# Performance work log

Measured on AMD Instinct MI355X. Metric: run time of the kernel, lower is better.

## Reference

```python
import jax, jax.numpy as jnp
import numpy as np

N = 50000      # nodes
E = 800000     # edges (before self-loops)
NFEAT = 128
NHID = 32
H = 8
NCLASS = 47
NEG_SLOPE = 0.2  # PyG GATv2Conv default


def gatv2_layer(x, src, dst, Wl, Wr, att, b, n):
    """One GATv2Conv layer (concat over heads). att: [H, C]."""
    h, c = att.shape
    xl = (x @ Wl).reshape(n, h, c)  # source transform (lin_l)
    xr = (x @ Wr).reshape(n, h, c)  # target transform (lin_r)
    e = jax.nn.leaky_relu(xl[src] + xr[dst], NEG_SLOPE)   # [E, H, C]
    logits = jnp.einsum('ehc,hc->eh', e, att)             # [E, H]
    # segment softmax over incoming edges of each target node
    m = jax.ops.segment_max(logits, dst, num_segments=n)  # [N, H]
    alpha = jnp.exp(logits - m[dst])
    denom = jax.ops.segment_sum(alpha, dst, num_segments=n)
    alpha = alpha / (denom[dst] + 1e-16)
    msg = xl[src] * alpha[:, :, None]                     # [E, H, C]
    out = jax.ops.segment_sum(msg, dst, num_segments=n)   # [N, H, C]
    return out.reshape(n, h * c) + b


def setup_inputs():
    key = jax.random.key(0)
    ks = jax.random.split(key, 16)
    s = 0.1
    x = jax.random.normal(ks[0], (N, NFEAT), jnp.float32)
    edge_index = jax.random.randint(ks[1], (2, E), 0, N)
    HID = H * NHID  # 256
    params = dict(
        Wl0=jax.random.normal(ks[2], (NFEAT, HID), jnp.float32) * s,
        Wr0=jax.random.normal(ks[3], (NFEAT, HID), jnp.float32) * s,
        a0=jax.random.normal(ks[4], (H, NHID), jnp.float32) * s,
        b0=jnp.zeros((HID,), jnp.float32),
        Wl1=jax.random.normal(ks[5], (HID, HID), jnp.float32) * s,
        Wr1=jax.random.normal(ks[6], (HID, HID), jnp.float32) * s,
        a1=jax.random.normal(ks[7], (H, NHID), jnp.float32) * s,
        b1=jnp.zeros((HID,), jnp.float32),
        Wl2=jax.random.normal(ks[8], (HID, NCLASS), jnp.float32) * s,
        Wr2=jax.random.normal(ks[9], (HID, NCLASS), jnp.float32) * s,
        a2=jax.random.normal(ks[10], (1, NCLASS), jnp.float32) * s,
        b2=jnp.zeros((NCLASS,), jnp.float32),
    )
    return {"x": x, "edge_index": edge_index, **params}


def reference(x, edge_index, Wl0, Wr0, a0, b0, Wl1, Wr1, a1, b1, Wl2, Wr2, a2, b2):
    n = x.shape[0]
    # PyG GATv2Conv adds self-loops by default
    loops = jnp.arange(n, dtype=edge_index.dtype)
    src = jnp.concatenate([edge_index[0], loops])
    dst = jnp.concatenate([edge_index[1], loops])
    h = gatv2_layer(x, src, dst, Wl0, Wr0, a0, b0, n)
    h = jax.nn.elu(h)
    h = gatv2_layer(h, src, dst, Wl1, Wr1, a1, b1, n)
    h = jax.nn.elu(h)
    h = gatv2_layer(h, src, dst, Wl2, Wr2, a2, b2, n)
    return jax.nn.log_softmax(h, axis=-1)
```

## Files before the change

### kernel.cpp

```cpp
#include <hip/hip_runtime.h>
#include <cmath>


#define NFEAT 128
#define HID 256
#define NCLS 47
#define L2PAD 64
#define LOG2E 1.44269504088896340736f

typedef __attribute__((ext_vector_type(8))) short bf16x8;
typedef __attribute__((ext_vector_type(4))) float f32x4;
typedef __attribute__((ext_vector_type(2))) float f32x2;

__device__ __forceinline__ unsigned short f2b(float f) {
  unsigned int u = __builtin_bit_cast(unsigned int, f);
  u += 0x7FFFu + ((u >> 16) & 1u);
  return (unsigned short)(u >> 16);
}
__device__ __forceinline__ float b2f(unsigned short s) {
  return __builtin_bit_cast(float, (unsigned int)s << 16);
}
__device__ __forceinline__ f32x2 b2f2(unsigned int u) {
  return (f32x2){__builtin_bit_cast(float, u << 16),
                 __builtin_bit_cast(float, u & 0xFFFF0000u)};
}
__device__ __forceinline__ void glds16(const unsigned short* g, unsigned short* l) {
  __builtin_amdgcn_global_load_lds(
      (const __attribute__((address_space(1))) unsigned int*)g,
      (__attribute__((address_space(3))) unsigned int*)l, 16, 0, 0);
}

__device__ __forceinline__ float quad_sum(float v) {
  int t = __builtin_amdgcn_mov_dpp(__builtin_bit_cast(int, v), 0xB1, 0xF, 0xF, true);
  v += __builtin_bit_cast(float, t);
  t = __builtin_amdgcn_mov_dpp(__builtin_bit_cast(int, v), 0x4E, 0xF, 0xF, true);
  v += __builtin_bit_cast(float, t);
  return v;
}

struct WtArgs {
  const float* W[6];
  unsigned short* WT[6];
  int K[6], M[6], off[6], total;
  const float* att;
  float* att48;
  int* deg;
  int n;
};
__global__ void k_wt_all(WtArgs a) {
  int i = blockIdx.x * blockDim.x + threadIdx.x;
  if (i >= a.total) {
    int j = i - a.total;
    if (j < 48) { a.att48[j] = (j < NCLS) ? a.att[j] * LOG2E : 0.f; return; }
    j -= 48;
    if (j < a.n) a.deg[j] = 1;
    return;
  }
  int s = 0;
  #pragma unroll
  for (int j = 1; j < 6; ++j) if (i >= a.off[j]) s = j;
  int jj = i - a.off[s];
  int K = a.K[s], M = a.M[s];
  int m = jj / K, k = jj - m * K;
  a.WT[s][jj] = (m < M) ? f2b(a.W[s][(size_t)k * M + m]) : (unsigned short)0;
}

__global__ void k_cast_count(const float* __restrict__ in,
                             unsigned short* __restrict__ out, int n4,
                             const int* __restrict__ dst,
                             int* __restrict__ deg, int e) {
  int i = blockIdx.x * blockDim.x + threadIdx.x;
  if (i < n4) {
    float4 v = reinterpret_cast<const float4*>(in)[i];
    ushort4 o = {f2b(v.x), f2b(v.y), f2b(v.z), f2b(v.w)};
    reinterpret_cast<ushort4*>(out)[i] = o;
  } else {
    int j = i - n4;
    if (j < e) atomicAdd(&deg[dst[j]], 1);
  }
}

__global__ __launch_bounds__(256) void k_bsum(const int* __restrict__ deg,
                                              int* __restrict__ bsum, int n) {
  int t = threadIdx.x;
  int base = blockIdx.x * 1024 + t * 4;
  int s = 0;
  if (base + 3 < n) {
    int4 v = *reinterpret_cast<const int4*>(deg + base);
    s = v.x + v.y + v.z + v.w;
  } else {
    for (int j = 0; j < 4; ++j) { int i = base + j; if (i < n) s += deg[i]; }
  }
  #pragma unroll
  for (int off = 1; off < 64; off <<= 1) s += __shfl_xor(s, off, 64);
  __shared__ int wsum[4];
  if ((t & 63) == 0) wsum[t >> 6] = s;
  __syncthreads();
  if (t == 0) bsum[blockIdx.x] = wsum[0] + wsum[1] + wsum[2] + wsum[3];
}

__global__ void k_scanb(int* __restrict__ bsum, int nb) {
  int lane = threadIdx.x;
  int v = (lane < nb) ? bsum[lane] : 0;
  #pragma unroll
  for (int off = 1; off < 64; off <<= 1) {
    int u = __shfl_up(v, off, 64);
    if (lane >= off) v += u;
  }
  if (lane < nb) bsum[lane] = v;
}

__global__ __launch_bounds__(256) void k_scanfinal(const int* __restrict__ deg,
                                                   const int* __restrict__ bscan,
                                                   int* __restrict__ rowptr,
                                                   int2* __restrict__ csr,
                                                   int* __restrict__ cursor, int n) {
  int t = threadIdx.x, b = blockIdx.x;
  int base = b * 1024 + t * 4;
  int v0 = 0, v1 = 0, v2 = 0, v3 = 0;
  if (base + 3 < n) {
    int4 v = *reinterpret_cast<const int4*>(deg + base);
    v0 = v.x; v1 = v.y; v2 = v.z; v3 = v.w;
  } else {
    if (base < n) v0 = deg[base];
    if (base + 1 < n) v1 = deg[base + 1];
    if (base + 2 < n) v2 = deg[base + 2];
    if (base + 3 < n) v3 = deg[base + 3];
  }
  int s = v0 + v1 + v2 + v3;
  int incl = s;
  #pragma unroll
  for (int off = 1; off < 64; off <<= 1) {
    int u = __shfl_up(incl, off, 64);
    if ((t & 63) >= off) incl += u;
  }
  __shared__ int wsum[4];
  int w = t >> 6, l = t & 63;
  if (l == 63) wsum[w] = incl;
  __syncthreads();
  int woff = 0;
  for (int j = 0; j < w; ++j) woff += wsum[j];
  int excl = incl - s + woff;
  int boff = (b == 0) ? 0 : bscan[b - 1];
  int p0 = boff + excl;
  int p1 = p0 + v0, p2 = p1 + v1, p3 = p2 + v2, p4 = p3 + v3;
  if (base < n)     { rowptr[base + 1] = p1; csr[p0] = make_int2(base, base);         cursor[base]     = p0 + 1; }
  if (base + 1 < n) { rowptr[base + 2] = p2; csr[p1] = make_int2(base + 1, base + 1); cursor[base + 1] = p1 + 1; }
  if (base + 2 < n) { rowptr[base + 3] = p3; csr[p2] = make_int2(base + 2, base + 2); cursor[base + 2] = p2 + 1; }
  if (base + 3 < n) { rowptr[base + 4] = p4; csr[p3] = make_int2(base + 3, base + 3); cursor[base + 3] = p3 + 1; }
  if (b == 0 && t == 0) rowptr[0] = 0;
}

__global__ void k_scatter(const int* __restrict__ src, const int* __restrict__ dst,
                          int* __restrict__ cursor, int2* __restrict__ csr, int e) {
  int i = blockIdx.x * blockDim.x + threadIdx.x;
  if (i < e) {
    int d = dst[i];
    int p = atomicAdd(&cursor[d], 1);
    csr[p] = make_int2(src[i], d);
  }
}

__global__ __launch_bounds__(512) void gemm_dual_bf16_128(
    const unsigned short* __restrict__ X, const unsigned short* __restrict__ WlT,
    const unsigned short* __restrict__ WrT, unsigned short* __restrict__ XL,
    unsigned short* __restrict__ XR, int N, int K, int Mpad) {
  __shared__ __align__(16) unsigned short S[3 * 128 * 64];
  unsigned short* Xs = S;
  unsigned short* Ls = S + 8192;
  unsigned short* Rs = S + 16384;

  const int t = threadIdx.x;
  const int col0 = blockIdx.x * 128;
  const int row0 = blockIdx.y * 128;
  const int w = t >> 6, lane = t & 63;
  const int wr = w >> 2, wc = w & 3;
  const int r15 = lane & 15, kc = lane >> 4;
  const bool tail = (row0 + 128 > N);

  const int row_a = t >> 3,          c16_a = t & 7;
  const int row_b = (t + 512) >> 3,  c16_b = t & 7;
  const int sg_a = (c16_a ^ (row_a & 7)) * 8;
  const int sg_b = (c16_b ^ (row_b & 7)) * 8;
  unsigned short* d0 = S + w * 512;
  unsigned short* d1 = S + 4096 + w * 512;

  f32x4 accL[4][2], accR[4][2];
  #pragma unroll
  for (int rf = 0; rf < 4; ++rf)
    #pragma unroll
    for (int cf = 0; cf < 2; ++cf) {
      accL[rf][cf] = (f32x4){0.f, 0.f, 0.f, 0.f};
      accR[rf][cf] = (f32x4){0.f, 0.f, 0.f, 0.f};
    }

  for (int k0 = 0; k0 < K; k0 += 64) {
    glds16(WlT + (size_t)(col0 + row_a) * K + k0 + sg_a, d0 + 8192);
    glds16(WlT + (size_t)(col0 + row_b) * K + k0 + sg_b, d1 + 8192);
    glds16(WrT + (size_t)(col0 + row_a) * K + k0 + sg_a, d0 + 16384);
    glds16(WrT + (size_t)(col0 + row_b) * K + k0 + sg_b, d1 + 16384);
    if (!tail) {
      glds16(X + (size_t)(row0 + row_a) * K + k0 + sg_a, d0);
      glds16(X + (size_t)(row0 + row_b) * K + k0 + sg_b, d1);
    } else {
      uint4 va = (uint4){0, 0, 0, 0}, vb = (uint4){0, 0, 0, 0};
      if (row0 + row_a < N)
        va = *reinterpret_cast<const uint4*>(X + (size_t)(row0 + row_a) * K + k0 + sg_a);
      if (row0 + row_b < N)
        vb = *reinterpret_cast<const uint4*>(X + (size_t)(row0 + row_b) * K + k0 + sg_b);
      *reinterpret_cast<uint4*>(Xs + row_a * 64 + c16_a * 8) = va;
      *reinterpret_cast<uint4*>(Xs + row_b * 64 + c16_b * 8) = vb;
    }
    __syncthreads();

    #pragma unroll
    for (int ks = 0; ks < 2; ++ks) {
      const int c16 = ks * 4 + kc;
      bf16x8 a[4];
      #pragma unroll
      for (int rf = 0; rf < 4; ++rf) {
        const int rA = wr * 64 + rf * 16 + r15;
        a[rf] = *reinterpret_cast<const bf16x8*>(Xs + rA * 64 + ((c16 ^ (rA & 7)) * 8));
      }
      #pragma unroll
      for (int cf = 0; cf < 2; ++cf) {
        const int rB = wc * 32 + cf * 16 + r15;
        const int so = rB * 64 + ((c16 ^ (rB & 7)) * 8);
        const bf16x8 bl = *reinterpret_cast<const bf16x8*>(Ls + so);
        const bf16x8 br = *reinterpret_cast<const bf16x8*>(Rs + so);
        #pragma unroll
        for (int rf = 0; rf < 4; ++rf) {
          accL[rf][cf] = __builtin_amdgcn_mfma_f32_16x16x32_bf16(a[rf], bl, accL[rf][cf], 0, 0, 0);
          accR[rf][cf] = __builtin_amdgcn_mfma_f32_16x16x32_bf16(a[rf], br, accR[rf][cf], 0, 0, 0);
        }
      }
    }
    __syncthreads();
  }

  #pragma unroll
  for (int rf = 0; rf < 4; ++rf) {
    #pragma unroll
    for (int cf = 0; cf < 2; ++cf) {
      int cc = col0 + wc * 32 + cf * 16 + r15;
      #pragma unroll
      for (int i = 0; i < 4; ++i) {
        int rr = row0 + wr * 64 + rf * 16 + kc * 4 + i;
        if (rr < N) {
          XL[(size_t)rr * Mpad + cc] = f2b(accL[rf][cf][i]);
          XR[(size_t)rr * Mpad + cc] = f2b(accR[rf][cf][i]);
        }
      }
    }
  }
}

__global__ __launch_bounds__(256) void gemm_dual_bf16(
    const unsigned short* __restrict__ X, const unsigned short* __restrict__ WlT,
    const unsigned short* __restrict__ WrT, unsigned short* __restrict__ XL,
    unsigned short* __restrict__ XR, int N, int K, int Mpad) {
  __shared__ __align__(16) unsigned short S[3 * 64 * 64];
  unsigned short* Xs = S;
  unsigned short* Ls = S + 4096;
  unsigned short* Rs = S + 8192;

  const int t = threadIdx.x;
  const int col0 = blockIdx.x * 64;
  const int row0 = blockIdx.y * 64;
  const int w = t >> 6, lane = t & 63;
  const int r15 = lane & 15, kc = lane >> 4;
  const bool tail = (row0 + 64 > N);

  const int rowa = t >> 3, c16a = t & 7;
  const int rowb = (t + 256) >> 3, c16b = t & 7;
  const int sga = (c16a ^ (rowa & 7)) * 8;
  const int sgb = (c16b ^ (rowb & 7)) * 8;
  unsigned short* ldst0 = S + (w * 512);
  unsigned short* ldst1 = S + (2048 + w * 512);

  f32x4 accL[4], accR[4];
  #pragma unroll
  for (int i = 0; i < 4; ++i) {
    accL[i] = (f32x4){0.f, 0.f, 0.f, 0.f};
    accR[i] = (f32x4){0.f, 0.f, 0.f, 0.f};
  }

  const int rA = 16 * w + r15;

  for (int k0 = 0; k0 < K; k0 += 64) {
    glds16(WlT + (size_t)(col0 + rowa) * K + k0 + sga, ldst0 + 4096);
    glds16(WlT + (size_t)(col0 + rowb) * K + k0 + sgb, ldst1 + 4096);
    glds16(WrT + (size_t)(col0 + rowa) * K + k0 + sga, ldst0 + 8192);
    glds16(WrT + (size_t)(col0 + rowb) * K + k0 + sgb, ldst1 + 8192);
    if (!tail) {
      glds16(X + (size_t)(row0 + rowa) * K + k0 + sga, ldst0);
      glds16(X + (size_t)(row0 + rowb) * K + k0 + sgb, ldst1);
    } else {
      uint4 va = (uint4){0, 0, 0, 0}, vb = (uint4){0, 0, 0, 0};
      if (row0 + rowa < N)
        va = *reinterpret_cast<const uint4*>(X + (size_t)(row0 + rowa) * K + k0 + sga);
      if (row0 + rowb < N)
        vb = *reinterpret_cast<const uint4*>(X + (size_t)(row0 + rowb) * K + k0 + sgb);
      *reinterpret_cast<uint4*>(Xs + rowa * 64 + c16a * 8) = va;
      *reinterpret_cast<uint4*>(Xs + rowb * 64 + c16b * 8) = vb;
    }
    __syncthreads();

    #pragma unroll
    for (int ks = 0; ks < 2; ++ks) {
      const int c16 = ks * 4 + kc;
      const bf16x8 a = *reinterpret_cast<const bf16x8*>(
          Xs + rA * 64 + ((c16 ^ (rA & 7)) * 8));
      #pragma unroll
      for (int nf = 0; nf < 4; ++nf) {
        const int rB = nf * 16 + r15;
        const int so = rB * 64 + ((c16 ^ (rB & 7)) * 8);
        const bf16x8 bl = *reinterpret_cast<const bf16x8*>(Ls + so);
        const bf16x8 br = *reinterpret_cast<const bf16x8*>(Rs + so);
        accL[nf] = __builtin_amdgcn_mfma_f32_16x16x32_bf16(a, bl, accL[nf], 0, 0, 0);
        accR[nf] = __builtin_amdgcn_mfma_f32_16x16x32_bf16(a, br, accR[nf], 0, 0, 0);
      }
    }
    __syncthreads();
  }

  #pragma unroll
  for (int nf = 0; nf < 4; ++nf) {
    int cc = col0 + nf * 16 + r15;
    #pragma unroll
    for (int i = 0; i < 4; ++i) {
      int rr = row0 + 16 * w + kc * 4 + i;
      if (rr < N) {
        XL[(size_t)rr * Mpad + cc] = f2b(accL[nf][i]);
        XR[(size_t)rr * Mpad + cc] = f2b(accR[nf][i]);
      }
    }
  }
}

__global__ __launch_bounds__(256) void gat_node_hc(
    const unsigned short* __restrict__ xl, const unsigned short* __restrict__ xr,
    const float* __restrict__ att, const float* __restrict__ bias,
    const int* __restrict__ rowptr, const int2* __restrict__ csr,
    unsigned short* __restrict__ out, int n) {
  int wid = (blockIdx.x * blockDim.x + threadIdx.x) >> 6;
  int lane = threadIdx.x & 63;
  if (wid >= n) return;
  const int q = lane & 31, half = lane >> 5;

  const uint4 xrp = *reinterpret_cast<const uint4*>(xr + (size_t)wid * HID + q * 8);
  const f32x2 xr2[4] = {b2f2(xrp.x), b2f2(xrp.y), b2f2(xrp.z), b2f2(xrp.w)};
  const float4 af0 = *reinterpret_cast<const float4*>(att + q * 8);
  const float4 af1 = *reinterpret_cast<const float4*>(att + q * 8 + 4);
  const f32x2 a2[4] = {{af0.x, af0.y}, {af0.z, af0.w},
                       {af1.x, af1.y}, {af1.z, af1.w}};

  float m = -1e30f, denom = 0.f;
  f32x2 acc[4] = {{0.f, 0.f}, {0.f, 0.f}, {0.f, 0.f}, {0.f, 0.f}};

  const int beg = rowptr[wid], end = rowptr[wid + 1];
  const int* csr_src = reinterpret_cast<const int*>(csr);
  for (int base = beg; base < end; base += 2) {
    const int i = base + half;
    const bool act = i < end;
    const int u = csr_src[2 * (act ? i : base)];
    const uint4 p = *reinterpret_cast<const uint4*>(xl + (size_t)u * HID + q * 8);
    const f32x2 x2[4] = {b2f2(p.x), b2f2(p.y), b2f2(p.z), b2f2(p.w)};
    f32x2 s2 = {0.f, 0.f};
    #pragma unroll
    for (int j = 0; j < 4; ++j) {
      f32x2 z = x2[j] + xr2[j];
      f32x2 lz = 0.2f * z;
      f32x2 r = {fmaxf(z.x, lz.x), fmaxf(z.y, lz.y)};
      s2 += r * a2[j];
    }
    float part = quad_sum(s2.x + s2.y);
    if (!act) part = -1e30f;
    if (__any(part > m + 8.f)) {
      float mn = fmaxf(m, part);
      float so = __expf(m - mn);
      float wn = act ? __expf(part - mn) : 0.f;
      denom = denom * so + wn;
      #pragma unroll
      for (int j = 0; j < 4; ++j) acc[j] = acc[j] * so + wn * x2[j];
      m = mn;
    } else {
      float wn = act ? __expf(part - m) : 0.f;
      denom += wn;
      #pragma unroll
      for (int j = 0; j < 4; ++j) acc[j] += wn * x2[j];
    }
  }

  float mo = __shfl_xor(m, 32, 64);
  float ms = fmaxf(m, mo);
  float sc = __expf(m - ms);
  denom *= sc;
  denom += __shfl_xor(denom, 32, 64);
  #pragma unroll
  for (int j = 0; j < 4; ++j) {
    acc[j] *= sc;
    acc[j].x += __shfl_xor(acc[j].x, 32, 64);
    acc[j].y += __shfl_xor(acc[j].y, 32, 64);
  }

  if (half == 0) {
    const float inv = 1.f / (denom + 1e-16f);
    const float4 bf0 = *reinterpret_cast<const float4*>(bias + q * 8);
    const float4 bf1 = *reinterpret_cast<const float4*>(bias + q * 8 + 4);
    float o[8] = {acc[0].x * inv + bf0.x, acc[0].y * inv + bf0.y,
                  acc[1].x * inv + bf0.z, acc[1].y * inv + bf0.w,
                  acc[2].x * inv + bf1.x, acc[2].y * inv + bf1.y,
                  acc[3].x * inv + bf1.z, acc[3].y * inv + bf1.w};
    #pragma unroll
    for (int j = 0; j < 8; ++j) o[j] = o[j] > 0.f ? o[j] : (__expf(o[j]) - 1.f);
    uint4 ov;
    ov.x = (unsigned)f2b(o[0]) | ((unsigned)f2b(o[1]) << 16);
    ov.y = (unsigned)f2b(o[2]) | ((unsigned)f2b(o[3]) << 16);
    ov.z = (unsigned)f2b(o[4]) | ((unsigned)f2b(o[5]) << 16);
    ov.w = (unsigned)f2b(o[6]) | ((unsigned)f2b(o[7]) << 16);
    *reinterpret_cast<uint4*>(out + (size_t)wid * HID + q * 8) = ov;
  }
}

__global__ __launch_bounds__(256) void k_logit_l2(
    const unsigned short* __restrict__ xl, const unsigned short* __restrict__ xr,
    const float* __restrict__ att48, const int2* __restrict__ csr,
    float* __restrict__ logit, int total) {
  int i = blockIdx.x * blockDim.x + threadIdx.x;
  if (i >= total) return;
  const int2 e = csr[i];
  const uint4* pu = reinterpret_cast<const uint4*>(xl + (size_t)e.x * L2PAD);
  const uint4* pv = reinterpret_cast<const uint4*>(xr + (size_t)e.y * L2PAD);
  f32x2 s2 = {0.f, 0.f};
  #pragma unroll
  for (int b = 0; b < 6; ++b) {
    const uint4 xu = pu[b], xv = pv[b];
    const f32x2* a2 = reinterpret_cast<const f32x2*>(att48 + b * 8);
    const unsigned ua[4] = {xu.x, xu.y, xu.z, xu.w};
    const unsigned va[4] = {xv.x, xv.y, xv.z, xv.w};
    #pragma unroll
    for (int j = 0; j < 4; ++j) {
      f32x2 z = b2f2(ua[j]) + b2f2(va[j]);
      f32x2 lz = 0.2f * z;
      f32x2 r = {fmaxf(z.x, lz.x), fmaxf(z.y, lz.y)};
      s2 += r * a2[j];
    }
  }
  logit[i] = s2.x + s2.y;
}

__global__ __launch_bounds__(256) void gat_node_l2(
    const unsigned short* __restrict__ xl, const float* __restrict__ logit,
    const float* __restrict__ bias, const int* __restrict__ rowptr,
    const int2* __restrict__ csr, float* __restrict__ out, int n) {
  int tid = blockIdx.x * blockDim.x + threadIdx.x;
  int node = tid >> 4;
  int q = threadIdx.x & 15;
  if (node >= n) return;
  const int c0 = 4 * q;
  const bool g0 = c0 < NCLS;
  const bool a1 = (c0 + 1) < NCLS, a2c = (c0 + 2) < NCLS, a3 = (c0 + 3) < NCLS;
  const int beg = rowptr[node], end = rowptr[node + 1];
  const int* csr_src = reinterpret_cast<const int*>(csr);

  float mx = -1e30f;
  for (int i = beg + q; i < end; i += 16) mx = fmaxf(mx, logit[i]);
  #pragma unroll
  for (int off = 1; off < 16; off <<= 1) mx = fmaxf(mx, __shfl_xor(mx, off, 64));

  float denom = 0.f;
  f32x2 acc0 = {0.f, 0.f}, acc1 = {0.f, 0.f};
  int i = beg;
  for (; i + 1 < end; i += 2) {
    const int u0 = csr_src[2 * i], u1 = csr_src[2 * (i + 1)];
    uint2 p0 = {0u, 0u}, p1 = {0u, 0u};
    if (g0) {
      p0 = *reinterpret_cast<const uint2*>(xl + (size_t)u0 * L2PAD + c0);
      p1 = *reinterpret_cast<const uint2*>(xl + (size_t)u1 * L2PAD + c0);
    }
    const float w0 = exp2f(logit[i] - mx);
    const float w1 = exp2f(logit[i + 1] - mx);
    denom += w0 + w1;
    acc0 += w0 * b2f2(p0.x) + w1 * b2f2(p1.x);
    acc1 += w0 * b2f2(p0.y) + w1 * b2f2(p1.y);
  }
  if (i < end) {
    const int u0 = csr_src[2 * i];
    uint2 p0 = {0u, 0u};
    if (g0) p0 = *reinterpret_cast<const uint2*>(xl + (size_t)u0 * L2PAD + c0);
    const float w0 = exp2f(logit[i] - mx);
    denom += w0;
    acc0 += w0 * b2f2(p0.x);
    acc1 += w0 * b2f2(p0.y);
  }

  const float inv = 1.f / (denom + 1e-16f);
  f32x2 r0 = acc0 * inv, r1 = acc1 * inv;
  if (g0)  r0.x += bias[c0];
  if (a1)  r0.y += bias[c0 + 1];
  if (a2c) r1.x += bias[c0 + 2];
  if (a3)  r1.y += bias[c0 + 3];

  float rm = -1e30f;
  if (g0)  rm = fmaxf(rm, r0.x);
  if (a1)  rm = fmaxf(rm, r0.y);
  if (a2c) rm = fmaxf(rm, r1.x);
  if (a3)  rm = fmaxf(rm, r1.y);
  #pragma unroll
  for (int off = 1; off < 16; off <<= 1) rm = fmaxf(rm, __shfl_xor(rm, off, 64));
  float se = 0.f;
  if (g0)  se += __expf(r0.x - rm);
  if (a1)  se += __expf(r0.y - rm);
  if (a2c) se += __expf(r1.x - rm);
  if (a3)  se += __expf(r1.y - rm);
  #pragma unroll
  for (int off = 1; off < 16; off <<= 1) se += __shfl_xor(se, off, 64);
  const float ls = rm + __logf(se);
  float* o = out + (size_t)node * NCLS;
  if (g0)  o[c0] = r0.x - ls;
  if (a1)  o[c0 + 1] = r0.y - ls;
  if (a2c) o[c0 + 2] = r1.x - ls;
  if (a3)  o[c0 + 3] = r1.y - ls;
}

extern "C" void kernel_launch(void* const* d_in, const int* in_sizes, int n_in,
                              void* d_out, int out_size, void* d_ws, size_t ws_size,
                              hipStream_t stream) {
  const float* x   = (const float*)d_in[0];
  const int* ei    = (const int*)d_in[1];
  const float* Wl0 = (const float*)d_in[2];
  const float* Wr0 = (const float*)d_in[3];
  const float* a0  = (const float*)d_in[4];
  const float* b0  = (const float*)d_in[5];
  const float* Wl1 = (const float*)d_in[6];
  const float* Wr1 = (const float*)d_in[7];
  const float* a1  = (const float*)d_in[8];
  const float* b1  = (const float*)d_in[9];
  const float* Wl2 = (const float*)d_in[10];
  const float* Wr2 = (const float*)d_in[11];
  const float* a2  = (const float*)d_in[12];
  const float* b2  = (const float*)d_in[13];

  const int N = in_sizes[0] / NFEAT;
  const int E = in_sizes[1] / 2;
  const int* src = ei;
  const int* dst = ei + E;
  const int total = E + N;

  char* ws = (char*)d_ws;
  unsigned short* xlb = (unsigned short*)ws; ws += (size_t)N * HID * 2;
  unsigned short* xrb = (unsigned short*)ws; ws += (size_t)N * HID * 2;
  unsigned short* xb  = (unsigned short*)ws; ws += (size_t)N * HID * 2;
  unsigned short* hb  = (unsigned short*)ws; ws += (size_t)N * HID * 2;
  unsigned short* WT  = (unsigned short*)ws; ws += (size_t)6 * HID * HID * 2;
  float* logit = (float*)ws; ws += (size_t)total * sizeof(float);
  float* att48 = (float*)ws; ws += 64 * sizeof(float);
  int* deg    = (int*)ws; ws += (size_t)N * sizeof(int);
  int* rowptr = (int*)ws; ws += (size_t)(N + 8) * sizeof(int);
  int* bsum   = (int*)ws; ws += (size_t)64 * sizeof(int);
  int2* csr   = (int2*)ws; ws += (size_t)total * sizeof(int2);

  unsigned short* WlT0 = WT + 0 * HID * HID;
  unsigned short* WrT0 = WT + 1 * HID * HID;
  unsigned short* WlT1 = WT + 2 * HID * HID;
  unsigned short* WrT1 = WT + 3 * HID * HID;
  unsigned short* WlT2 = WT + 4 * HID * HID;
  unsigned short* WrT2 = WT + 5 * HID * HID;

  const int TB = 256;
  const int nbScan = (N + 1023) / 1024;
  const int n4 = N * NFEAT / 4;

  {
    WtArgs a;
    const float* Wsrc[6] = {Wl0, Wr0, Wl1, Wr1, Wl2, Wr2};
    unsigned short* Wdst[6] = {WlT0, WrT0, WlT1, WrT1, WlT2, WrT2};
    int Ks[6] = {NFEAT, NFEAT, HID, HID, HID, HID};
    int Ms[6] = {HID, HID, HID, HID, NCLS, NCLS};
    int Mp[6] = {HID, HID, HID, HID, L2PAD, L2PAD};
    int off = 0;
    for (int s = 0; s < 6; ++s) {
      a.W[s] = Wsrc[s]; a.WT[s] = Wdst[s]; a.K[s] = Ks[s]; a.M[s] = Ms[s];
      a.off[s] = off; off += Mp[s] * Ks[s];
    }
    a.total = off;
    a.att = a2; a.att48 = att48;
    a.deg = deg; a.n = N;
    k_wt_all<<<(a.total + 48 + N + TB - 1) / TB, TB, 0, stream>>>(a);
  }
  k_cast_count<<<(n4 + E + TB - 1) / TB, TB, 0, stream>>>(x, xb, n4, dst, deg, E);

  k_bsum<<<nbScan, TB, 0, stream>>>(deg, bsum, N);
  k_scanb<<<1, 64, 0, stream>>>(bsum, nbScan);
  k_scanfinal<<<nbScan, TB, 0, stream>>>(deg, bsum, rowptr, csr, deg, N);
  k_scatter<<<(E + TB - 1) / TB, TB, 0, stream>>>(src, dst, deg, csr, E);

  const int nodeBlocks = (N + 3) / 4;
  const int rb128 = (N + 127) / 128;
  const int rb64 = (N + 63) / 64;
  const int l2Blocks = (N + 15) / 16;

  {
    dim3 g(HID / 128, rb128);
    gemm_dual_bf16_128<<<g, 512, 0, stream>>>(xb, WlT0, WrT0, xlb, xrb, N, NFEAT, HID);
    gat_node_hc<<<nodeBlocks, 256, 0, stream>>>(xlb, xrb, a0, b0, rowptr, csr, hb, N);
  }
  {
    dim3 g(HID / 128, rb128);
    gemm_dual_bf16_128<<<g, 512, 0, stream>>>(hb, WlT1, WrT1, xlb, xrb, N, HID, HID);
    gat_node_hc<<<nodeBlocks, 256, 0, stream>>>(xlb, xrb, a1, b1, rowptr, csr, xb, N);
  }
  {
    dim3 g(1, rb64);
    gemm_dual_bf16<<<g, 256, 0, stream>>>(xb, WlT2, WrT2, xlb, xrb, N, HID, L2PAD);
    k_logit_l2<<<(total + TB - 1) / TB, TB, 0, stream>>>(xlb, xrb, att48, csr,
                                                         logit, total);
    gat_node_l2<<<l2Blocks, 256, 0, stream>>>(xlb, logit, b2, rowptr, csr,
                                              (float*)d_out, N);
  }
}
```

Baseline: 361.2 us.

## Split GATv2 hidden-layer attention into separate logit kernel and two-pass softmax aggregation

Moves per-edge, per-head logit computation out of the node aggregation kernel into a new edge-parallel kernel that writes [E,8] fp32 logits (pre-scaled by log2e). The node kernel then does a max pass over stored logits and a simple exp2-weighted accumulation, dropping the online-softmax rescaling and divergent branches. This costs an extra kernel launch per layer and writes and rereads a roughly 27MB logit buffer, and the logit kernel gathers xl rows a second time.

```diff
diff --git a/kernel.cpp b/kernel.cpp
--- a/kernel.cpp
+++ b/kernel.cpp
@@ -29,12 +29,11 @@
       (const __attribute__((address_space(1))) unsigned int*)g,
       (__attribute__((address_space(3))) unsigned int*)l, 16, 0, 0);
 }
-
-__device__ __forceinline__ float quad_sum(float v) {
+__device__ __forceinline__ float quad_max(float v) {
   int t = __builtin_amdgcn_mov_dpp(__builtin_bit_cast(int, v), 0xB1, 0xF, 0xF, true);
-  v += __builtin_bit_cast(float, t);
+  v = fmaxf(v, __builtin_bit_cast(float, t));
   t = __builtin_amdgcn_mov_dpp(__builtin_bit_cast(int, v), 0x4E, 0xF, 0xF, true);
-  v += __builtin_bit_cast(float, t);
+  v = fmaxf(v, __builtin_bit_cast(float, t));
   return v;
 }
 
@@ -338,68 +337,73 @@
   }
 }
 
+__global__ __launch_bounds__(256) void k_logit_hc(
+    const unsigned short* __restrict__ xl, const unsigned short* __restrict__ xr,
+    const float* __restrict__ att, const int2* __restrict__ csr,
+    float* __restrict__ logit8, int total) {
+  int idx = blockIdx.x * blockDim.x + threadIdx.x;
+  int e = idx >> 3, h = idx & 7;
+  if (e >= total) return;
+  const int2 ed = csr[e];
+  const uint4* pl = reinterpret_cast<const uint4*>(xl + (size_t)ed.x * HID + h * 32);
+  const uint4* pr = reinterpret_cast<const uint4*>(xr + (size_t)ed.y * HID + h * 32);
+  const f32x2* a2 = reinterpret_cast<const f32x2*>(att + h * 32);
+  f32x2 s2 = {0.f, 0.f};
+  #pragma unroll
+  for (int b = 0; b < 4; ++b) {
+    const uint4 xu = pl[b], xv = pr[b];
+    const unsigned ua[4] = {xu.x, xu.y, xu.z, xu.w};
+    const unsigned va[4] = {xv.x, xv.y, xv.z, xv.w};
+    #pragma unroll
+    for (int j = 0; j < 4; ++j) {
+      f32x2 z = b2f2(ua[j]) + b2f2(va[j]);
+      f32x2 lz = 0.2f * z;
+      f32x2 r = {fmaxf(z.x, lz.x), fmaxf(z.y, lz.y)};
+      s2 += r * a2[b * 4 + j];
+    }
+  }
+  logit8[idx] = (s2.x + s2.y) * LOG2E;
+}
+
 __global__ __launch_bounds__(256) void gat_node_hc(
-    const unsigned short* __restrict__ xl, const unsigned short* __restrict__ xr,
-    const float* __restrict__ att, const float* __restrict__ bias,
-    const int* __restrict__ rowptr, const int2* __restrict__ csr,
-    unsigned short* __restrict__ out, int n) {
+    const unsigned short* __restrict__ xl, const float* __restrict__ logit8,
+    const float* __restrict__ bias, const int* __restrict__ rowptr,
+    const int2* __restrict__ csr, unsigned short* __restrict__ out, int n) {
   int wid = (blockIdx.x * blockDim.x + threadIdx.x) >> 6;
   int lane = threadIdx.x & 63;
   if (wid >= n) return;
   const int q = lane & 31, half = lane >> 5;
-
-  const uint4 xrp = *reinterpret_cast<const uint4*>(xr + (size_t)wid * HID + q * 8);
-  const f32x2 xr2[4] = {b2f2(xrp.x), b2f2(xrp.y), b2f2(xrp.z), b2f2(xrp.w)};
-  const float4 af0 = *reinterpret_cast<const float4*>(att + q * 8);
-  const float4 af1 = *reinterpret_cast<const float4*>(att + q * 8 + 4);
-  const f32x2 a2[4] = {{af0.x, af0.y}, {af0.z, af0.w},
-                       {af1.x, af1.y}, {af1.z, af1.w}};
-
-  float m = -1e30f, denom = 0.f;
-  f32x2 acc[4] = {{0.f, 0.f}, {0.f, 0.f}, {0.f, 0.f}, {0.f, 0.f}};
+  const int h = q >> 2;
 
   const int beg = rowptr[wid], end = rowptr[wid + 1];
   const int* csr_src = reinterpret_cast<const int*>(csr);
+
+  float mx = -1e30f;
+  for (int i = beg + (q & 3); i < end; i += 4)
+    mx = fmaxf(mx, logit8[8 * i + h]);
+  mx = quad_max(mx);
+
+  float denom = 0.f;
+  f32x2 acc[4] = {{0.f, 0.f}, {0.f, 0.f}, {0.f, 0.f}, {0.f, 0.f}};
+
   for (int base = beg; base < end; base += 2) {
     const int i = base + half;
     const bool act = i < end;
-    const int u = csr_src[2 * (act ? i : base)];
+    const int ii = act ? i : base;
+    const int u = csr_src[2 * ii];
     const uint4 p = *reinterpret_cast<const uint4*>(xl + (size_t)u * HID + q * 8);
-    const f32x2 x2[4] = {b2f2(p.x), b2f2(p.y), b2f2(p.z), b2f2(p.w)};
-    f32x2 s2 = {0.f, 0.f};
-    #pragma unroll
-    for (int j = 0; j < 4; ++j) {
-      f32x2 z = x2[j] + xr2[j];
-      f32x2 lz = 0.2f * z;
-      f32x2 r = {fmaxf(z.x, lz.x), fmaxf(z.y, lz.y)};
-      s2 += r * a2[j];
-    }
-    float part = quad_sum(s2.x + s2.y);
-    if (!act) part = -1e30f;
-    if (__any(part > m + 8.f)) {
-      float mn = fmaxf(m, part);
-      float so = __expf(m - mn);
-      float wn = act ? __expf(part - mn) : 0.f;
-      denom = denom * so + wn;
-      #pragma unroll
-      for (int j = 0; j < 4; ++j) acc[j] = acc[j] * so + wn * x2[j];
-      m = mn;
-    } else {
-      float wn = act ? __expf(part - m) : 0.f;
-      denom += wn;
-      #pragma unroll
-      for (int j = 0; j < 4; ++j) acc[j] += wn * x2[j];
-    }
-  }
-
-  float mo = __shfl_xor(m, 32, 64);
-  float ms = fmaxf(m, mo);
-  float sc = __expf(m - ms);
-  denom *= sc;
+    float w = exp2f(logit8[8 * ii + h] - mx);
+    if (!act) w = 0.f;
+    denom += w;
+    acc[0] += w * b2f2(p.x);
+    acc[1] += w * b2f2(p.y);
+    acc[2] += w * b2f2(p.z);
+    acc[3] += w * b2f2(p.w);
+  }
+
   denom += __shfl_xor(denom, 32, 64);
   #pragma unroll
   for (int j = 0; j < 4; ++j) {
-    acc[j] *= sc;
     acc[j].x += __shfl_xor(acc[j].x, 32, 64);
     acc[j].y += __shfl_xor(acc[j].y, 32, 64);
   }
@@ -554,7 +558,7 @@
   unsigned short* xb  = (unsigned short*)ws; ws += (size_t)N * HID * 2;
   unsigned short* hb  = (unsigned short*)ws; ws += (size_t)N * HID * 2;
   unsigned short* WT  = (unsigned short*)ws; ws += (size_t)6 * HID * HID * 2;
-  float* logit = (float*)ws; ws += (size_t)total * sizeof(float);
+  float* logit8 = (float*)ws; ws += (size_t)total * 8 * sizeof(float);
   float* att48 = (float*)ws; ws += 64 * sizeof(float);
   int* deg    = (int*)ws; ws += (size_t)N * sizeof(int);
   int* rowptr = (int*)ws; ws += (size_t)(N + 8) * sizeof(int);
@@ -600,23 +604,26 @@
   const int rb128 = (N + 127) / 128;
   const int rb64 = (N + 63) / 64;
   const int l2Blocks = (N + 15) / 16;
+  const int lgBlocks = ((total * 8) + TB - 1) / TB;
 
   {
     dim3 g(HID / 128, rb128);
     gemm_dual_bf16_128<<<g, 512, 0, stream>>>(xb, WlT0, WrT0, xlb, xrb, N, NFEAT, HID);
-    gat_node_hc<<<nodeBlocks, 256, 0, stream>>>(xlb, xrb, a0, b0, rowptr, csr, hb, N);
+    k_logit_hc<<<lgBlocks, TB, 0, stream>>>(xlb, xrb, a0, csr, logit8, total);
+    gat_node_hc<<<nodeBlocks, 256, 0, stream>>>(xlb, logit8, b0, rowptr, csr, hb, N);
   }
   {
     dim3 g(HID / 128, rb128);
     gemm_dual_bf16_128<<<g, 512, 0, stream>>>(hb, WlT1, WrT1, xlb, xrb, N, HID, HID);
-    gat_node_hc<<<nodeBlocks, 256, 0, stream>>>(xlb, xrb, a1, b1, rowptr, csr, xb, N);
+    k_logit_hc<<<lgBlocks, TB, 0, stream>>>(xlb, xrb, a1, csr, logit8, total);
+    gat_node_hc<<<nodeBlocks, 256, 0, stream>>>(xlb, logit8, b1, rowptr, csr, xb, N);
   }
   {
     dim3 g(1, rb64);
     gemm_dual_bf16<<<g, 256, 0, stream>>>(xb, WlT2, WrT2, xlb, xrb, N, HID, L2PAD);
     k_logit_l2<<<(total + TB - 1) / TB, TB, 0, stream>>>(xlb, xrb, att48, csr,
-                                                         logit, total);
-    gat_node_l2<<<l2Blocks, 256, 0, stream>>>(xlb, logit, b2, rowptr, csr,
+                                                         logit8, total);
+    gat_node_l2<<<l2Blocks, 256, 0, stream>>>(xlb, logit8, b2, rowptr, csr,
                                               (float*)d_out, N);
   }
 }
```

New measurement: 645.4 us. 78.7% more time.
